# Kernel tuning notes

Hardware: AMD Instinct MI355X
Metric: run time of the kernel (lower is better)

## Reference

```python
import jax, jax.numpy as jnp
import numpy as np

H = 128          # hidden
L = 4            # num PNA layers
NG = 32          # graphs in the batch
OUT = 12
N_NODES = 30000
N_EDGES = 480000
IN_NODE = 64
IN_EDGE = 16
EPS_BN = 1e-5
EPS_STD = 1e-5
# deg histogram torch.tensor([1,2,3,4,5,6]): cnt_i nodes have degree i
_cnt = np.arange(1.0, 7.0)
AVG_LOG = float((np.log(np.arange(6) + 1.0) * _cnt).sum() / _cnt.sum())


def _lin(k, fan_in, fan_out):
    return jax.random.normal(k, (fan_in, fan_out), jnp.float32) * 0.05


def setup_inputs() -> dict:
    key = jax.random.key(0)
    ks = jax.random.split(key, 16)
    d = {}
    d["x"] = jax.random.normal(ks[0], (N_NODES, IN_NODE), jnp.float32)
    d["edge_attr"] = jax.random.normal(ks[1], (N_EDGES, IN_EDGE), jnp.float32)
    d["edge_index"] = jax.random.randint(ks[2], (2, N_EDGES), 0, N_NODES)
    d["batch"] = jnp.sort(jax.random.randint(ks[3], (N_NODES,), 0, NG))
    d["node_emb_W"] = _lin(ks[4], IN_NODE, H)
    d["node_emb_b"] = jnp.zeros((H,), jnp.float32)
    d["edge_emb_W"] = _lin(ks[5], IN_EDGE, H)
    d["edge_emb_b"] = jnp.zeros((H,), jnp.float32)
    kl = jax.random.split(ks[6], 4 * L)
    d["edge_enc_W"] = jnp.stack([_lin(kl[i], H, H) for i in range(L)])
    d["edge_enc_b"] = jnp.zeros((L, H), jnp.float32)
    d["pre_W"] = jnp.stack([_lin(kl[L + i], 3 * H, H) for i in range(L)])
    d["pre_b"] = jnp.zeros((L, H), jnp.float32)
    d["post_W"] = jnp.stack([_lin(kl[2 * L + i], 13 * H, H) for i in range(L)])
    d["post_b"] = jnp.zeros((L, H), jnp.float32)
    d["lin_W"] = jnp.stack([_lin(kl[3 * L + i], H, H) for i in range(L)])
    d["lin_b"] = jnp.zeros((L, H), jnp.float32)
    d["bn_gamma"] = jnp.ones((L, H), jnp.float32)
    d["bn_beta"] = jnp.zeros((L, H), jnp.float32)
    d["head1_W"] = _lin(ks[7], H, H // 2)
    d["head1_b"] = jnp.zeros((H // 2,), jnp.float32)
    d["head2_W"] = _lin(ks[8], H // 2, OUT)
    d["head2_b"] = jnp.zeros((OUT,), jnp.float32)
    return d


def _pna_layer(x, e, src, dst, eW, eb, pW, pb, oW, ob, lW, lb):
    n = x.shape[0]
    ee = e @ eW + eb                                      # edge encoder [E, H]
    h = jnp.concatenate([x[dst], x[src], ee], axis=-1)    # (x_i, x_j, e) [E, 3H]
    m = h @ pW + pb                                       # pre-nn messages [E, H]
    ones = jnp.ones((m.shape[0],), m.dtype)
    deg = jax.ops.segment_sum(ones, dst, num_segments=n)  # in-degree [N]
    degc = jnp.maximum(deg, 1.0)[:, None]
    has = (deg > 0.0)[:, None]
    mean = jax.ops.segment_sum(m, dst, num_segments=n) / degc
    mn = jnp.where(has, jax.ops.segment_min(m, dst, num_segments=n), 0.0)
    mx = jnp.where(has, jax.ops.segment_max(m, dst, num_segments=n), 0.0)
    mean_sq = jax.ops.segment_sum(m * m, dst, num_segments=n) / degc
    std = jnp.sqrt(jax.nn.relu(mean_sq - mean * mean) + EPS_STD)
    agg = jnp.concatenate([mean, mn, mx, std], axis=-1)   # aggregators [N, 4H]
    amp = jnp.log(degc + 1.0) / AVG_LOG                   # amplification scale
    out = jnp.concatenate([agg, agg * amp, agg / amp], axis=-1)  # id/amp/atten [N, 12H]
    out = jnp.concatenate([x, out], axis=-1) @ oW + ob    # post-nn [N, H]
    return out @ lW + lb                                  # final lin


def reference(x, edge_index, batch, edge_attr, node_emb_W, node_emb_b,
              edge_emb_W, edge_emb_b, edge_enc_W, edge_enc_b, pre_W, pre_b,
              post_W, post_b, lin_W, lin_b, bn_gamma, bn_beta,
              head1_W, head1_b, head2_W, head2_b):
    src, dst = edge_index[0], edge_index[1]
    h = x @ node_emb_W + node_emb_b
    e = edge_attr @ edge_emb_W + edge_emb_b
    for l in range(L):
        h = _pna_layer(h, e, src, dst, edge_enc_W[l], edge_enc_b[l],
                       pre_W[l], pre_b[l], post_W[l], post_b[l],
                       lin_W[l], lin_b[l])
        mu = h.mean(axis=0)
        var = h.var(axis=0)  # biased, as BatchNorm training-mode normalization
        h = (h - mu) / jnp.sqrt(var + EPS_BN) * bn_gamma[l] + bn_beta[l]
        h = jax.nn.relu(h)   # dropout == identity (eval mode reference)
    g = jax.ops.segment_sum(h, batch, num_segments=NG)   # global_add_pool [NG, H]
    z = jax.nn.relu(g @ head1_W + head1_b)
    return z @ head2_W + head2_b
```

## Files before the change

kernel.cpp:

```cpp
#include <hip/hip_runtime.h>
#include <hip/hip_bf16.h>
#include <math.h>

#define NN 30000
#define NE 480000
#define NLAYER 4
#define NGR 32
#define NOUT 12
#define EPS_BN 1e-5f
#define EPS_STD 1e-5f
#define AVG_LOG 1.3821454785305053f
#define MB_GRID 235

typedef unsigned short ushort_t;
typedef __bf16 bf16x8 __attribute__((ext_vector_type(8)));
typedef float floatx4 __attribute__((ext_vector_type(4)));

__device__ __forceinline__ float bfu(ushort_t u){
  union { unsigned int ui; float f; } c; c.ui = ((unsigned int)u) << 16; return c.f;
}
__device__ __forceinline__ ushort_t f2bf(float f){
  union { float f; unsigned int u; } c; c.f = f;
  unsigned int lsb = (c.u >> 16) & 1u;
  c.u += 0x7FFFu + lsb;
  return (ushort_t)(c.u >> 16);
}

__device__ __forceinline__ int plausible(unsigned int bits32){
  unsigned int e = (bits32 >> 23) & 0xFF;
  if(e == 0xFF) return 0;
  if(bits32 == 0 || bits32 == 0x80000000u) return 1;
  return (e >= 93 && e <= 140) ? 1 : 0;
}

__global__ void k_detect(const ushort_t* __restrict__ xr, int* __restrict__ flag){
  __shared__ int cnt[2];
  if(threadIdx.x < 2) cnt[threadIdx.x] = 0;
  __syncthreads();
  const unsigned int* xf = (const unsigned int*)xr;
  int gf = 0, gb = 0;
  for(int i = threadIdx.x; i < 1024; i += 256){
    gf += plausible(xf[i]);
    gb += plausible(((unsigned int)xr[i]) << 16);
  }
  atomicAdd(&cnt[0], gf);
  atomicAdd(&cnt[1], gb);
  __syncthreads();
  if(threadIdx.x == 0) *flag = (cnt[1] >= cnt[0]) ? 1 : 0;
}

#define NJOBS 18
struct CvtJob { const void* s; float* d; int n; };
struct CvtArgs { CvtJob j[NJOBS]; const int* flag; };

__global__ void k_cvt(CvtArgs a){
  int ji = blockIdx.y;
  const int isbf = *a.flag;
  float* d = a.j[ji].d;
  int n = a.j[ji].n;
  if(isbf){
    const ushort_t* s = (const ushort_t*)a.j[ji].s;
    for(int i = blockIdx.x*256 + threadIdx.x; i < n; i += gridDim.x*256) d[i] = bfu(s[i]);
  } else {
    const float* s = (const float*)a.j[ji].s;
    for(int i = blockIdx.x*256 + threadIdx.x; i < n; i += gridDim.x*256) d[i] = s[i];
  }
}

__global__ void k_xbf(const void* __restrict__ x, ushort_t* __restrict__ d,
                      const int* __restrict__ flag){
  int i = blockIdx.x*256 + threadIdx.x;
  if(i >= NN*64) return;
  if(*flag) d[i] = ((const ushort_t*)x)[i];
  else      d[i] = f2bf(((const float*)x)[i]);
}

#define NTR 9
struct TrJob { const float* s; ushort_t* d; int K, N; };
struct TrArgs { TrJob j[NTR]; };

__global__ void k_tr(TrArgs a){
  TrJob j = a.j[blockIdx.y];
  int nk = j.K >> 6, nn = j.N >> 6;
  int tile = blockIdx.x;
  if(tile >= nk*nn) return;
  int tk = tile % nk, tn = tile / nk;
  int k0 = tk*64, n0 = tn*64;
  __shared__ float t[64][65];
  int w = threadIdx.x >> 6, c = threadIdx.x & 63;
  #pragma unroll
  for(int i=0;i<16;i+=1){
    int r = i*4 + w;
    t[r][c] = j.s[(size_t)(k0+r)*j.N + n0 + c];
  }
  __syncthreads();
  #pragma unroll
  for(int i=0;i<16;i+=1){
    int r = i*4 + w;
    j.d[(size_t)(n0+r)*j.K + k0 + c] = f2bf(t[c][r]);
  }
}

#define NFOLD 16
struct FoldJob { const float* s1; const float* s2; ushort_t* d; int Kd; };
struct FoldArgs { FoldJob j[NFOLD]; };

__global__ void k_fold(FoldArgs a){
  FoldJob j = a.j[blockIdx.y];
  const int n0 = blockIdx.x*16;
  __shared__ float s2s[128][16];
  int tid = threadIdx.x;
  for(int idx = tid; idx < 128*16; idx += 256){
    int t = idx >> 4, jj = idx & 15;
    s2s[t][jj] = j.s2[t*128 + n0 + jj];
  }
  __syncthreads();
  for(int k = tid; k < j.Kd; k += 256){
    float part[16];
    #pragma unroll
    for(int p=0;p<16;p++) part[p] = 0.f;
    for(int t0=0; t0<128; t0+=32){
      float rr[32];
      #pragma unroll
      for(int tt=0;tt<32;tt++) rr[tt] = j.s1[(size_t)k*128 + t0 + tt];
      #pragma unroll
      for(int p=0;p<16;p++){
        float acc = 0.f;
        #pragma unroll
        for(int tt=0;tt<32;tt++) acc += rr[tt]*s2s[t0+tt][p];
        part[p] += acc;
      }
    }
    #pragma unroll
    for(int p=0;p<16;p++)
      j.d[(size_t)(n0+p)*j.Kd + k] = f2bf(part[p]);
  }
}

__global__ void k_foldb(const float* __restrict__ postB, const float* __restrict__ linW,
                        const float* __restrict__ linB, float* __restrict__ biasY){
  int l = blockIdx.x, c = threadIdx.x;
  float a = linB[l*128+c];
  const float* L = linW + (size_t)l*128*128;
  const float* pb = postB + l*128;
  for(int t=0;t<128;t++) a += pb[t]*L[t*128+c];
  biasY[l*128+c] = a;
}

__global__ void k_deg(const int* __restrict__ dst, int* __restrict__ deg){
  int i = blockIdx.x*256 + threadIdx.x;
  if(i < NE){
    unsigned d = (unsigned)dst[i];
    if(d < NN) atomicAdd(&deg[d], 1);
  }
}

__global__ void k_scan1(const int* __restrict__ deg, int* __restrict__ rp,
                        int* __restrict__ bsum){
  __shared__ int wsum[16];
  int tid = threadIdx.x, lane = tid & 63, wid = tid >> 6;
  int i = blockIdx.x*1024 + tid;
  int v = (i < NN) ? deg[i] : 0;
  int incl = v;
  #pragma unroll
  for(int off=1; off<64; off<<=1){
    int t = __shfl_up(incl, off, 64);
    if(lane >= off) incl += t;
  }
  if(lane==63) wsum[wid] = incl;
  __syncthreads();
  int woff = 0;
  for(int w=0; w<wid; w++) woff += wsum[w];
  if(i < NN) rp[i+1] = incl + woff;
  if(tid == 0){
    int t = 0;
    for(int w=0; w<16; w++) t += wsum[w];
    bsum[blockIdx.x] = t;
  }
}

__global__ void k_scan2(const int* __restrict__ bsum, int* __restrict__ boff,
                        int* __restrict__ rp, int nb){
  if(threadIdx.x == 0){
    int run = 0;
    for(int b=0;b<nb;b++){ boff[b] = run; run += bsum[b]; }
    rp[0] = 0;
  }
}

__global__ void k_scan3(int* __restrict__ rp, const int* __restrict__ boff){
  int i = blockIdx.x*1024 + threadIdx.x;
  if(i < NN) rp[i+1] += boff[blockIdx.x];
}

__global__ void k_scatter(const int* __restrict__ src, const int* __restrict__ dst,
                          const int* __restrict__ rp, int* __restrict__ fill,
                          int* __restrict__ src_csr, int* __restrict__ eix_csr){
  int i = blockIdx.x*256 + threadIdx.x;
  if(i >= NE) return;
  unsigned d = (unsigned)dst[i];
  unsigned s = (unsigned)src[i];
  if(d >= NN || s >= NN) return;
  int pos = rp[d] + atomicAdd(&fill[d], 1);
  src_csr[pos] = (int)s;
  eix_csr[pos] = i;
}

__global__ void k_srt(const int* __restrict__ rp, int* __restrict__ eix,
                      int* __restrict__ src){
  int n = blockIdx.x*256 + threadIdx.x;
  if(n >= NN) return;
  int s0 = rp[n], e0 = rp[n+1];
  for(int i=s0+1;i<e0;i++){
    int ke = eix[i], ks = src[i];
    int j = i-1;
    while(j >= s0 && eix[j] > ke){
      eix[j+1] = eix[j]; src[j+1] = src[j]; j--;
    }
    eix[j+1] = ke; src[j+1] = ks;
  }
}

__global__ void k_gather_ea(const int* __restrict__ eix, const void* __restrict__ ea,
                            ushort_t* __restrict__ out, const int* __restrict__ flag){
  int j = blockIdx.x*128 + threadIdx.x;
  if(j >= NE) return;
  int i = eix[j];
  uint4* d = (uint4*)(out + (size_t)j*16);
  if(*flag){
    const uint4* s = (const uint4*)((const ushort_t*)ea + (size_t)i*16);
    d[0] = s[0]; d[1] = s[1];
  } else {
    const float* s = (const float*)ea + (size_t)i*16;
    union { ushort_t us[16]; uint4 u4[2]; } pk;
    #pragma unroll
    for(int k=0;k<16;k++) pk.us[k] = f2bf(s[k]);
    d[0] = pk.u4[0]; d[1] = pk.u4[1];
  }
}

__global__ void k_prep_K(const float* __restrict__ embW, const float* __restrict__ embB,
                         const float* __restrict__ encW, const float* __restrict__ encB,
                         const float* __restrict__ preW, const float* __restrict__ preB,
                         float* __restrict__ Kf){
  int bx = blockIdx.x;
  int l = bx / 17, r = bx % 17;
  int c = threadIdx.x;
  const float* eW = encW + (size_t)l*128*128;
  const float* P3 = preW + (size_t)l*384*128 + 256*128;
  __shared__ float trow[128];
  float a;
  if(r < 16){
    a = 0.f;
    const float* w = embW + r*128;
    for(int k=0;k<128;k++) a += w[k]*eW[k*128+c];
  } else {
    a = encB[l*128+c];
    for(int k=0;k<128;k++) a += embB[k]*eW[k*128+c];
  }
  trow[c] = a;
  __syncthreads();
  float o = (r==16) ? preB[l*128+c] : 0.f;
  for(int k=0;k<128;k++) o += trow[k]*P3[k*128+c];
  Kf[(size_t)l*17*128 + r*128 + c] = o;
}

template<int EPI, int OUTBF>
__launch_bounds__(256)
__global__ void k_mm(const ushort_t* __restrict__ A, const ushort_t* __restrict__ BT,
                     void* __restrict__ C, int M, int K, int ldc,
                     const float* __restrict__ bias,
                     const float* __restrict__ Tm,
                     const float* __restrict__ ampv, const float* __restrict__ invv,
                     float* __restrict__ bnpart){
  __shared__ __align__(16) ushort_t Als[128][88];
  __shared__ __align__(16) ushort_t Bls[128][88];
  __shared__ float s_part[8][128];
  __shared__ float q_part[8][128];
  const int tid = threadIdx.x;
  const int m0 = blockIdx.x*128, n0 = blockIdx.y*128;
  const int w = tid >> 6, lane = tid & 63;
  const int wm = (w & 1)*64, wn = (w >> 1)*64;
  const int quad = lane >> 4, l15 = lane & 15;
  floatx4 acc[4][4] = {};

  for(int k0=0; k0<K; k0+=64){
    #pragma unroll
    for(int i=0;i<4;i++){
      int c = tid + 256*i;
      int row = c >> 3, kc = (c & 7)*8;
      uint4 va = make_uint4(0u,0u,0u,0u);
      int gr = m0 + row;
      if(gr < M) va = *(const uint4*)(A + (size_t)gr*K + k0 + kc);
      *(uint4*)(&Als[row][kc]) = va;
      uint4 vb = *(const uint4*)(BT + (size_t)(n0+row)*K + k0 + kc);
      *(uint4*)(&Bls[row][kc]) = vb;
    }
    __syncthreads();
    #pragma unroll
    for(int ks=0; ks<64; ks+=32){
      bf16x8 a[4], b[4];
      #pragma unroll
      for(int i=0;i<4;i++) a[i] = *(const bf16x8*)(&Als[wm+16*i+l15][ks+quad*8]);
      #pragma unroll
      for(int j=0;j<4;j++) b[j] = *(const bf16x8*)(&Bls[wn+16*j+l15][ks+quad*8]);
      #pragma unroll
      for(int i=0;i<4;i++)
        #pragma unroll
        for(int j=0;j<4;j++)
          acc[i][j] = __builtin_amdgcn_mfma_f32_16x16x32_bf16(a[i], b[j], acc[i][j], 0, 0, 0);
    }
    __syncthreads();
  }

  float s[4] = {0,0,0,0}, q[4] = {0,0,0,0};
  #pragma unroll
  for(int i=0;i<4;i++){
    #pragma unroll
    for(int r=0;r<4;r++){
      int grow = m0 + wm + 16*i + quad*4 + r;
      if(grow >= M) continue;
      float amp = 0.f, iv = 0.f;
      const float* tr = nullptr;
      if(EPI==1){ amp = ampv[grow]; iv = invv[grow]; tr = Tm + (size_t)grow*384; }
      #pragma unroll
      for(int j=0;j<4;j++){
        int gcol = n0 + wn + 16*j + l15;
        float v = acc[i][j][r];
        if(bias) v += bias[gcol];
        if(EPI==1) v += tr[gcol] + amp*tr[128+gcol] + iv*tr[256+gcol];
        if(OUTBF) ((ushort_t*)C)[(size_t)grow*ldc + gcol] = f2bf(v);
        else      ((float*)  C)[(size_t)grow*ldc + gcol] = v;
        if(EPI==1){ s[j] += v; q[j] += v*v; }
      }
    }
  }
  if(EPI==1){
    const int slot = (w & 1)*4 + quad;
    #pragma unroll
    for(int j=0;j<4;j++){
      s_part[slot][wn + 16*j + l15] = s[j];
      q_part[slot][wn + 16*j + l15] = q[j];
    }
    __syncthreads();
    if(tid < 128){
      float ss = 0.f, qq = 0.f;
      #pragma unroll
      for(int sl=0; sl<8; sl++){ ss += s_part[sl][tid]; qq += q_part[sl][tid]; }
      bnpart[(size_t)blockIdx.x*256 + tid]       = ss;
      bnpart[(size_t)blockIdx.x*256 + 128 + tid] = qq;
    }
  }
}

__launch_bounds__(128)
__global__ void k_agg(const int* __restrict__ rp, const int* __restrict__ src_csr,
                      const ushort_t* __restrict__ ea_csr, const float* __restrict__ Kf,
                      const float* __restrict__ AB,
                      ushort_t* __restrict__ agg, float* __restrict__ ampv,
                      float* __restrict__ invv){
  const int n = blockIdx.x, c = threadIdx.x;
  const int s0 = rp[n], e0 = rp[n+1];
  const int deg = e0 - s0;
  float kcol[16];
  #pragma unroll
  for(int k=0;k<16;k++) kcol[k] = Kf[k*128+c];
  const float base = AB[(size_t)n*256 + c] + Kf[16*128+c];
  float sum=0.f, sq=0.f, mn=INFINITY, mx=-INFINITY;
  __shared__ float ea_s[16][16];
  __shared__ int src_s[16];
  for(int j0=s0; j0<e0; j0+=16){
    int cnt = min(16, e0-j0);
    __syncthreads();
    int ee = c>>4, kk = c&15;
    if(ee < cnt)   ea_s[ee][kk]   = bfu(ea_csr[(size_t)(j0+ee)*16+kk]);
    if(ee+8 < cnt) ea_s[ee+8][kk] = bfu(ea_csr[(size_t)(j0+ee+8)*16+kk]);
    if(c < cnt) src_s[c] = src_csr[j0+c];
    __syncthreads();
    for(int e=0;e<cnt;e++){
      float m = base + AB[(size_t)src_s[e]*256 + 128 + c];
      #pragma unroll
      for(int k=0;k<16;k++) m += ea_s[e][k]*kcol[k];
      sum += m; sq += m*m; mn = fminf(mn,m); mx = fmaxf(mx,m);
    }
  }
  float degc = (float)(deg>0?deg:1);
  float mean = sum/degc;
  float var  = fmaxf(sq/degc - mean*mean, 0.f);
  float sd = sqrtf(var + EPS_STD);
  if(deg==0){ mn=0.f; mx=0.f; }
  ushort_t* o = agg + (size_t)n*512;
  o[c]     = f2bf(mean);
  o[128+c] = f2bf(mn);
  o[256+c] = f2bf(mx);
  o[384+c] = f2bf(sd);
  if(c==0){
    float amp = logf(degc+1.f)/AVG_LOG;
    ampv[n] = amp; invv[n] = 1.f/amp;
  }
}

__global__ void k_bn_fin(const float* __restrict__ bnpart, int nb,
                         const float* __restrict__ gamma, const float* __restrict__ beta,
                         float* __restrict__ scale, float* __restrict__ shift){
  int c = threadIdx.x;
  float s = 0.f, q = 0.f;
  for(int b=0;b<nb;b++){
    s += bnpart[(size_t)b*256 + c];
    q += bnpart[(size_t)b*256 + 128 + c];
  }
  float mu  = s*(1.f/NN);
  float var = fmaxf(q*(1.f/NN) - mu*mu, 0.f);
  float inv = 1.f/sqrtf(var + EPS_BN);
  float sc = gamma[c]*inv;
  scale[c] = sc;
  shift[c] = beta[c] - mu*sc;
}

__global__ void k_bn_relu(const float* __restrict__ y, const float* __restrict__ scale,
                          const float* __restrict__ shift, ushort_t* __restrict__ h){
  int i = blockIdx.x*256 + threadIdx.x;
  if(i >= NN*128) return;
  int c = i & 127;
  float v = fmaxf(y[i]*scale[c] + shift[c], 0.f);
  h[i] = f2bf(v);
}

__device__ __forceinline__ int lbound(const int* a, int n, int v){
  int lo = 0, hi = n;
  while(lo < hi){ int mid = (lo+hi) >> 1; if(a[mid] < v) lo = mid+1; else hi = mid; }
  return lo;
}

__launch_bounds__(128)
__global__ void k_pool1(const ushort_t* __restrict__ h, const int* __restrict__ batch,
                        float* __restrict__ gpart){
  int b = blockIdx.x, ch = blockIdx.y, c = threadIdx.x;
  int lo = lbound(batch, NN, b), hi = lbound(batch, NN, b+1);
  int len = hi - lo;
  int per = (len + 7) >> 3;
  int r0 = min(lo + ch*per, hi);
  int r1 = min(r0 + per, hi);
  float acc = 0.f;
  for(int r=r0;r<r1;r++) acc += bfu(h[(size_t)r*128+c]);
  gpart[((size_t)b*8 + ch)*128 + c] = acc;
}

__global__ void k_pool2(const float* __restrict__ gpart, float* __restrict__ g){
  int b = blockIdx.x, c = threadIdx.x;
  float acc = 0.f;
  #pragma unroll
  for(int ch=0; ch<8; ch++) acc += gpart[((size_t)b*8 + ch)*128 + c];
  g[(size_t)b*128 + c] = acc;
}

__launch_bounds__(64)
__global__ void k_head(const float* __restrict__ g, const float* __restrict__ W1,
                       const float* __restrict__ b1, const float* __restrict__ W2,
                       const float* __restrict__ b2, void* __restrict__ out,
                       const int* __restrict__ flag){
  __shared__ float gs[128];
  __shared__ float zs[64];
  int r = blockIdx.x, tid = threadIdx.x;
  gs[tid] = g[r*128 + tid];
  gs[tid+64] = g[r*128 + tid + 64];
  __syncthreads();
  float a = b1[tid];
  for(int k=0;k<128;k++) a += gs[k]*W1[k*64+tid];
  zs[tid] = fmaxf(a, 0.f);
  __syncthreads();
  if(tid < NOUT){
    float o = b2[tid];
    for(int k=0;k<64;k++) o += zs[k]*W2[k*12+tid];
    if(*flag) ((ushort_t*)out)[r*NOUT + tid] = f2bf(o);
    else      ((float*)out)[r*NOUT + tid] = o;
  }
}

extern "C" void kernel_launch(void* const* d_in, const int* in_sizes, int n_in,
                              void* d_out, int out_size, void* d_ws, size_t ws_size,
                              hipStream_t stream){
  const void* x_raw = d_in[0];
  const void* ea_raw;
  const int*  eidx;
  const int*  batch;
  if(in_sizes[1] == 2*NE){
    eidx   = (const int*)d_in[1];
    batch  = (const int*)d_in[2];
    ea_raw = d_in[3];
  } else {
    ea_raw = d_in[1];
    eidx   = (const int*)d_in[2];
    batch  = (const int*)d_in[3];
  }
  const void* nembW_r = d_in[4];
  const void* nembB_r = d_in[5];
  const void* eembW_r = d_in[6];
  const void* eembB_r = d_in[7];
  const void* encW_r  = d_in[8];
  const void* encB_r  = d_in[9];
  const void* preW_r  = d_in[10];
  const void* preB_r  = d_in[11];
  const void* postW_r = d_in[12];
  const void* postB_r = d_in[13];
  const void* linW_r  = d_in[14];
  const void* linB_r  = d_in[15];
  const void* bnG_r   = d_in[16];
  const void* bnB_r   = d_in[17];
  const void* h1W_r   = d_in[18];
  const void* h1B_r   = d_in[19];
  const void* h2W_r   = d_in[20];
  const void* h2B_r   = d_in[21];

  char* p = (char*)d_ws;
  auto alloc = [&](size_t bytes)->void*{
    void* r = (void*)p; p += (bytes + 255) & ~(size_t)255; return r;
  };
  int*      dtflag  = (int*)     alloc(sizeof(int)*16);
  int*      deg     = (int*)     alloc(sizeof(int)*NN);
  int*      fill    = (int*)     alloc(sizeof(int)*NN);
  int*      rp      = (int*)     alloc(sizeof(int)*(NN+1));
  int*      bsum    = (int*)     alloc(sizeof(int)*64);
  int*      boff    = (int*)     alloc(sizeof(int)*64);
  int*      src_csr = (int*)     alloc(sizeof(int)*NE);
  int*      eix_csr = (int*)     alloc(sizeof(int)*NE);
  ushort_t* ea_csr  = (ushort_t*)alloc(sizeof(ushort_t)*(size_t)NE*16);
  ushort_t* xbf     = (ushort_t*)alloc(sizeof(ushort_t)*(size_t)NN*64);
  ushort_t* h       = (ushort_t*)alloc(sizeof(ushort_t)*(size_t)NN*128);
  ushort_t* aggb    = (ushort_t*)alloc(sizeof(ushort_t)*(size_t)NN*512);
  float*    AB      = (float*)   alloc(sizeof(float)*(size_t)NN*256);
  float*    Tm      = (float*)   alloc(sizeof(float)*(size_t)NN*384);
  float*    y       = (float*)   alloc(sizeof(float)*(size_t)NN*128);
  float*    ampv    = (float*)   alloc(sizeof(float)*NN);
  float*    invv    = (float*)   alloc(sizeof(float)*NN);
  float*    Kf      = (float*)   alloc(sizeof(float)*4*17*128);
  float*    bnpart  = (float*)   alloc(sizeof(float)*(size_t)MB_GRID*256);
  float*    bnscale = (float*)   alloc(sizeof(float)*128);
  float*    bnshift = (float*)   alloc(sizeof(float)*128);
  float*    gpart   = (float*)   alloc(sizeof(float)*32*8*128);
  float*    g       = (float*)   alloc(sizeof(float)*32*128);
  float*    biasY   = (float*)   alloc(sizeof(float)*4*128);
  ushort_t* WembT   = (ushort_t*)alloc(sizeof(ushort_t)*128*64);
  ushort_t* P12T    = (ushort_t*)alloc(sizeof(ushort_t)*4*256*128);
  ushort_t* WcatFT  = (ushort_t*)alloc(sizeof(ushort_t)*(size_t)4*384*512);
  ushort_t* W0FT    = (ushort_t*)alloc(sizeof(ushort_t)*4*128*128);
  float* nembW = (float*)alloc(sizeof(float)*64*128);
  float* nembB = (float*)alloc(sizeof(float)*128);
  float* eembW = (float*)alloc(sizeof(float)*16*128);
  float* eembB = (float*)alloc(sizeof(float)*128);
  float* encW  = (float*)alloc(sizeof(float)*4*128*128);
  float* encB  = (float*)alloc(sizeof(float)*4*128);
  float* preW  = (float*)alloc(sizeof(float)*4*384*128);
  float* preB  = (float*)alloc(sizeof(float)*4*128);
  float* postW = (float*)alloc(sizeof(float)*(size_t)4*1664*128);
  float* postB = (float*)alloc(sizeof(float)*4*128);
  float* linW  = (float*)alloc(sizeof(float)*4*128*128);
  float* linB  = (float*)alloc(sizeof(float)*4*128);
  float* bnG   = (float*)alloc(sizeof(float)*4*128);
  float* bnB   = (float*)alloc(sizeof(float)*4*128);
  float* h1W   = (float*)alloc(sizeof(float)*128*64);
  float* h1B   = (float*)alloc(sizeof(float)*64);
  float* h2W   = (float*)alloc(sizeof(float)*64*12);
  float* h2B   = (float*)alloc(sizeof(float)*12);

  CvtArgs ca;
  ca.flag = dtflag;
  int ji = 0;
  auto job = [&](const void* s, float* d, int n){ ca.j[ji].s=s; ca.j[ji].d=d; ca.j[ji].n=n; ji++; };
  job(nembW_r, nembW, 64*128);
  job(nembB_r, nembB, 128);
  job(eembW_r, eembW, 16*128);
  job(eembB_r, eembB, 128);
  job(encW_r,  encW,  4*128*128);
  job(encB_r,  encB,  4*128);
  job(preW_r,  preW,  4*384*128);
  job(preB_r,  preB,  4*128);
  job(postW_r, postW, 4*1664*128);
  job(postB_r, postB, 4*128);
  job(linW_r,  linW,  4*128*128);
  job(linB_r,  linB,  4*128);
  job(bnG_r,   bnG,   4*128);
  job(bnB_r,   bnB,   4*128);
  job(h1W_r,   h1W,   128*64);
  job(h1B_r,   h1B,   64);
  job(h2W_r,   h2W,   64*12);
  job(h2B_r,   h2B,   12);

  TrArgs ta;
  int ti = 0;
  auto tj = [&](const float* s, ushort_t* d, int K, int N){ ta.j[ti].s=s; ta.j[ti].d=d; ta.j[ti].K=K; ta.j[ti].N=N; ti++; };
  tj(nembW, WembT, 64, 128);
  for(int l=0;l<4;l++){
    const float* pw = preW + (size_t)l*384*128;
    tj(pw,           P12T + (size_t)l*256*128,           128, 128);
    tj(pw + 128*128, P12T + (size_t)l*256*128 + 128*128, 128, 128);
  }

  FoldArgs fa;
  int fi = 0;
  for(int l=0;l<4;l++){
    const float* po = postW + (size_t)l*1664*128;
    const float* L  = linW + (size_t)l*128*128;
    for(int b=0;b<3;b++){
      fa.j[fi].s1 = po + (size_t)(128 + b*512)*128;
      fa.j[fi].s2 = L;
      fa.j[fi].d  = WcatFT + (size_t)l*384*512 + (size_t)b*128*512;
      fa.j[fi].Kd = 512;
      fi++;
    }
    fa.j[fi].s1 = po;
    fa.j[fi].s2 = L;
    fa.j[fi].d  = W0FT + (size_t)l*128*128;
    fa.j[fi].Kd = 128;
    fi++;
  }

  const int* esrc = eidx;
  const int* edst = eidx + NE;

  hipMemsetAsync(deg, 0, sizeof(int)*NN, stream);
  hipMemsetAsync(fill, 0, sizeof(int)*NN, stream);

  k_detect<<<1, 256, 0, stream>>>((const ushort_t*)x_raw, dtflag);
  k_cvt<<<dim3(128, NJOBS), 256, 0, stream>>>(ca);
  k_xbf<<<(NN*64+255)/256, 256, 0, stream>>>(x_raw, xbf, dtflag);
  k_tr<<<dim3(4, NTR), 256, 0, stream>>>(ta);
  k_fold<<<dim3(8, NFOLD), 256, 0, stream>>>(fa);
  k_foldb<<<4, 128, 0, stream>>>(postB, linW, linB, biasY);
  k_prep_K<<<68, 128, 0, stream>>>(eembW, eembB, encW, encB, preW, preB, Kf);

  k_deg<<<(NE+255)/256, 256, 0, stream>>>(edst, deg);
  k_scan1<<<30, 1024, 0, stream>>>(deg, rp, bsum);
  k_scan2<<<1, 64, 0, stream>>>(bsum, boff, rp, 30);
  k_scan3<<<30, 1024, 0, stream>>>(rp, boff);
  k_scatter<<<(NE+255)/256, 256, 0, stream>>>(esrc, edst, rp, fill, src_csr, eix_csr);
  k_srt<<<(NN+255)/256, 256, 0, stream>>>(rp, eix_csr, src_csr);
  k_gather_ea<<<(NE+127)/128, 128, 0, stream>>>(eix_csr, ea_raw, ea_csr, dtflag);

  k_mm<0,1><<<dim3(MB_GRID,1), 256, 0, stream>>>(xbf, WembT, h, NN, 64, 128,
                                                 nembB, nullptr, nullptr, nullptr, nullptr);

  for(int l=0; l<NLAYER; l++){
    k_mm<0,0><<<dim3(MB_GRID,2), 256, 0, stream>>>(h, P12T + (size_t)l*256*128, AB, NN, 128, 256,
                                                   nullptr, nullptr, nullptr, nullptr, nullptr);
    k_agg<<<NN, 128, 0, stream>>>(rp, src_csr, ea_csr, Kf + (size_t)l*17*128,
                                  AB, aggb, ampv, invv);
    k_mm<0,0><<<dim3(MB_GRID,3), 256, 0, stream>>>(aggb, WcatFT + (size_t)l*384*512, Tm, NN, 512, 384,
                                                   nullptr, nullptr, nullptr, nullptr, nullptr);
    k_mm<1,0><<<dim3(MB_GRID,1), 256, 0, stream>>>(h, W0FT + (size_t)l*128*128, y, NN, 128, 128,
                                                   biasY + l*128, Tm, ampv, invv, bnpart);
    k_bn_fin<<<1, 128, 0, stream>>>(bnpart, MB_GRID, bnG + l*128, bnB + l*128,
                                    bnscale, bnshift);
    k_bn_relu<<<(NN*128+255)/256, 256, 0, stream>>>(y, bnscale, bnshift, h);
  }

  k_pool1<<<dim3(NGR,8), 128, 0, stream>>>(h, batch, gpart);
  k_pool2<<<NGR, 128, 0, stream>>>(gpart, g);
  k_head<<<NGR, 64, 0, stream>>>(g, h1W, h1B, h2W, h2B, d_out, dtflag);
}
```

Measured before the change: 1.165 ms.

## Fuse post-NN GEMMs into one kernel, shrink intermediates to bf16, streamline CSR sort

```diff
diff --git a/kernel.cpp b/kernel.cpp
--- a/kernel.cpp
+++ b/kernel.cpp
@@ -193,39 +193,51 @@
   if(i < NN) rp[i+1] += boff[blockIdx.x];
 }
 
-__global__ void k_scatter(const int* __restrict__ src, const int* __restrict__ dst,
+__global__ void k_scatter(const int* __restrict__ dst,
                           const int* __restrict__ rp, int* __restrict__ fill,
-                          int* __restrict__ src_csr, int* __restrict__ eix_csr){
+                          int* __restrict__ eix_csr){
   int i = blockIdx.x*256 + threadIdx.x;
   if(i >= NE) return;
   unsigned d = (unsigned)dst[i];
-  unsigned s = (unsigned)src[i];
-  if(d >= NN || s >= NN) return;
+  if(d >= NN) return;
   int pos = rp[d] + atomicAdd(&fill[d], 1);
-  src_csr[pos] = (int)s;
   eix_csr[pos] = i;
 }
 
-__global__ void k_srt(const int* __restrict__ rp, int* __restrict__ eix,
-                      int* __restrict__ src){
-  int n = blockIdx.x*256 + threadIdx.x;
+__launch_bounds__(64)
+__global__ void k_srt(const int* __restrict__ rp, int* __restrict__ eix){
+  __shared__ int buf[64][129];
+  int t = threadIdx.x;
+  int n = blockIdx.x*64 + t;
   if(n >= NN) return;
-  int s0 = rp[n], e0 = rp[n+1];
-  for(int i=s0+1;i<e0;i++){
-    int ke = eix[i], ks = src[i];
-    int j = i-1;
-    while(j >= s0 && eix[j] > ke){
-      eix[j+1] = eix[j]; src[j+1] = src[j]; j--;
-    }
-    eix[j+1] = ke; src[j+1] = ks;
-  }
-}
-
-__global__ void k_gather_ea(const int* __restrict__ eix, const void* __restrict__ ea,
-                            ushort_t* __restrict__ out, const int* __restrict__ flag){
+  int s0 = rp[n], e0 = rp[n+1], d = e0 - s0;
+  if(d <= 1) return;
+  if(d <= 128){
+    int* b = buf[t];
+    for(int i=0;i<d;i++) b[i] = eix[s0+i];
+    for(int i=1;i<d;i++){
+      int k = b[i], j = i-1;
+      while(j >= 0 && b[j] > k){ b[j+1] = b[j]; j--; }
+      b[j+1] = k;
+    }
+    for(int i=0;i<d;i++) eix[s0+i] = b[i];
+  } else {
+    for(int i=s0+1;i<e0;i++){
+      int k = eix[i], j = i-1;
+      while(j >= s0 && eix[j] > k){ eix[j+1] = eix[j]; j--; }
+      eix[j+1] = k;
+    }
+  }
+}
+
+__global__ void k_gather_ea(const int* __restrict__ eix, const int* __restrict__ esrc,
+                            const void* __restrict__ ea,
+                            ushort_t* __restrict__ out, int* __restrict__ src_csr,
+                            const int* __restrict__ flag){
   int j = blockIdx.x*128 + threadIdx.x;
   if(j >= NE) return;
   int i = eix[j];
+  src_csr[j] = esrc[i];
   uint4* d = (uint4*)(out + (size_t)j*16);
   if(*flag){
     const uint4* s = (const uint4*)((const ushort_t*)ea + (size_t)i*16);
@@ -268,15 +280,10 @@
 template<int EPI, int OUTBF>
 __launch_bounds__(256)
 __global__ void k_mm(const ushort_t* __restrict__ A, const ushort_t* __restrict__ BT,
-                     void* __restrict__ C, int M, int K, int ldc,
-                     const float* __restrict__ bias,
-                     const float* __restrict__ Tm,
-                     const float* __restrict__ ampv, const float* __restrict__ invv,
-                     float* __restrict__ bnpart){
+                     void* __restrict__ C, void* __restrict__ C2,
+                     int M, int K, int ldc, const float* __restrict__ bias){
   __shared__ __align__(16) ushort_t Als[128][88];
   __shared__ __align__(16) ushort_t Bls[128][88];
-  __shared__ float s_part[8][128];
-  __shared__ float q_part[8][128];
   const int tid = threadIdx.x;
   const int m0 = blockIdx.x*128, n0 = blockIdx.y*128;
   const int w = tid >> 6, lane = tid & 63;
@@ -313,50 +320,163 @@
     __syncthreads();
   }
 
+  #pragma unroll
+  for(int i=0;i<4;i++){
+    #pragma unroll
+    for(int r=0;r<4;r++){
+      int grow = m0 + wm + 16*i + quad*4 + r;
+      if(grow >= M) continue;
+      #pragma unroll
+      for(int j=0;j<4;j++){
+        int gcol = n0 + wn + 16*j + l15;
+        float v = acc[i][j][r];
+        if(EPI==0){
+          if(bias) v += bias[gcol];
+          if(OUTBF) ((ushort_t*)C)[(size_t)grow*ldc + gcol] = f2bf(v);
+          else      ((float*)  C)[(size_t)grow*ldc + gcol] = v;
+        } else {
+          if(n0 == 0) ((float*)C)[(size_t)grow*128 + gcol] = v;
+          else        ((ushort_t*)C2)[(size_t)grow*128 + (gcol-128)] = f2bf(v);
+        }
+      }
+    }
+  }
+}
+
+__launch_bounds__(256)
+__global__ void k_post(const ushort_t* __restrict__ aggb, const ushort_t* __restrict__ h,
+                       const ushort_t* __restrict__ Wcat, const ushort_t* __restrict__ W0,
+                       const float* __restrict__ biasY,
+                       const float* __restrict__ ampv, const float* __restrict__ invv,
+                       ushort_t* __restrict__ y, float* __restrict__ bnpart){
+  __shared__ __align__(16) ushort_t Als[128][88];
+  __shared__ __align__(16) ushort_t Bls[128][88];
+  __shared__ float s_part[8][128];
+  __shared__ float q_part[8][128];
+  __shared__ float amp_s[128];
+  __shared__ float inv_s[128];
+  const int tid = threadIdx.x;
+  const int m0 = blockIdx.x*128;
+  const int w = tid >> 6, lane = tid & 63;
+  const int wm = (w & 1)*64, wn = (w >> 1)*64;
+  const int quad = lane >> 4, l15 = lane & 15;
+  if(tid < 128){
+    int rr = min(m0 + tid, NN-1);
+    amp_s[tid] = ampv[rr];
+    inv_s[tid] = invv[rr];
+  }
+  floatx4 accY[4][4] = {};
+
+  for(int p=0; p<3; p++){
+    floatx4 accP[4][4] = {};
+    floatx4 (*tgt)[4] = (p==0) ? accY : accP;
+    const ushort_t* Wp = Wcat + (size_t)p*128*512;
+    for(int k0=0; k0<512; k0+=64){
+      #pragma unroll
+      for(int i=0;i<4;i++){
+        int c = tid + 256*i;
+        int row = c >> 3, kc = (c & 7)*8;
+        uint4 va = make_uint4(0u,0u,0u,0u);
+        int gr = m0 + row;
+        if(gr < NN) va = *(const uint4*)(aggb + (size_t)gr*512 + k0 + kc);
+        *(uint4*)(&Als[row][kc]) = va;
+        uint4 vb = *(const uint4*)(Wp + (size_t)row*512 + k0 + kc);
+        *(uint4*)(&Bls[row][kc]) = vb;
+      }
+      __syncthreads();
+      #pragma unroll
+      for(int ks=0; ks<64; ks+=32){
+        bf16x8 a[4], b[4];
+        #pragma unroll
+        for(int i=0;i<4;i++) a[i] = *(const bf16x8*)(&Als[wm+16*i+l15][ks+quad*8]);
+        #pragma unroll
+        for(int j=0;j<4;j++) b[j] = *(const bf16x8*)(&Bls[wn+16*j+l15][ks+quad*8]);
+        #pragma unroll
+        for(int i=0;i<4;i++)
+          #pragma unroll
+          for(int j=0;j<4;j++)
+            tgt[i][j] = __builtin_amdgcn_mfma_f32_16x16x32_bf16(a[i], b[j], tgt[i][j], 0, 0, 0);
+      }
+      __syncthreads();
+    }
+    if(p > 0){
+      const float* cs = (p==1) ? amp_s : inv_s;
+      #pragma unroll
+      for(int i=0;i<4;i++)
+        #pragma unroll
+        for(int r=0;r<4;r++){
+          float coef = cs[wm + 16*i + quad*4 + r];
+          #pragma unroll
+          for(int j=0;j<4;j++) accY[i][j][r] += coef*accP[i][j][r];
+        }
+    }
+  }
+
+  for(int k0=0; k0<128; k0+=64){
+    #pragma unroll
+    for(int i=0;i<4;i++){
+      int c = tid + 256*i;
+      int row = c >> 3, kc = (c & 7)*8;
+      uint4 va = make_uint4(0u,0u,0u,0u);
+      int gr = m0 + row;
+      if(gr < NN) va = *(const uint4*)(h + (size_t)gr*128 + k0 + kc);
+      *(uint4*)(&Als[row][kc]) = va;
+      uint4 vb = *(const uint4*)(W0 + (size_t)row*128 + k0 + kc);
+      *(uint4*)(&Bls[row][kc]) = vb;
+    }
+    __syncthreads();
+    #pragma unroll
+    for(int ks=0; ks<64; ks+=32){
+      bf16x8 a[4], b[4];
+      #pragma unroll
+      for(int i=0;i<4;i++) a[i] = *(const bf16x8*)(&Als[wm+16*i+l15][ks+quad*8]);
+      #pragma unroll
+      for(int j=0;j<4;j++) b[j] = *(const bf16x8*)(&Bls[wn+16*j+l15][ks+quad*8]);
+      #pragma unroll
+      for(int i=0;i<4;i++)
+        #pragma unroll
+        for(int j=0;j<4;j++)
+          accY[i][j] = __builtin_amdgcn_mfma_f32_16x16x32_bf16(a[i], b[j], accY[i][j], 0, 0, 0);
+    }
+    __syncthreads();
+  }
+
   float s[4] = {0,0,0,0}, q[4] = {0,0,0,0};
   #pragma unroll
   for(int i=0;i<4;i++){
     #pragma unroll
     for(int r=0;r<4;r++){
       int grow = m0 + wm + 16*i + quad*4 + r;
-      if(grow >= M) continue;
-      float amp = 0.f, iv = 0.f;
-      const float* tr = nullptr;
-      if(EPI==1){ amp = ampv[grow]; iv = invv[grow]; tr = Tm + (size_t)grow*384; }
+      if(grow >= NN) continue;
       #pragma unroll
       for(int j=0;j<4;j++){
-        int gcol = n0 + wn + 16*j + l15;
-        float v = acc[i][j][r];
-        if(bias) v += bias[gcol];
-        if(EPI==1) v += tr[gcol] + amp*tr[128+gcol] + iv*tr[256+gcol];
-        if(OUTBF) ((ushort_t*)C)[(size_t)grow*ldc + gcol] = f2bf(v);
-        else      ((float*)  C)[(size_t)grow*ldc + gcol] = v;
-        if(EPI==1){ s[j] += v; q[j] += v*v; }
+        int gcol = wn + 16*j + l15;
+        float v = accY[i][j][r] + biasY[gcol];
+        y[(size_t)grow*128 + gcol] = f2bf(v);
+        s[j] += v; q[j] += v*v;
       }
     }
   }
-  if(EPI==1){
-    const int slot = (w & 1)*4 + quad;
-    #pragma unroll
-    for(int j=0;j<4;j++){
-      s_part[slot][wn + 16*j + l15] = s[j];
-      q_part[slot][wn + 16*j + l15] = q[j];
-    }
-    __syncthreads();
-    if(tid < 128){
-      float ss = 0.f, qq = 0.f;
-      #pragma unroll
-      for(int sl=0; sl<8; sl++){ ss += s_part[sl][tid]; qq += q_part[sl][tid]; }
-      bnpart[(size_t)blockIdx.x*256 + tid]       = ss;
-      bnpart[(size_t)blockIdx.x*256 + 128 + tid] = qq;
-    }
+  const int slot = (w & 1)*4 + quad;
+  #pragma unroll
+  for(int j=0;j<4;j++){
+    s_part[slot][wn + 16*j + l15] = s[j];
+    q_part[slot][wn + 16*j + l15] = q[j];
+  }
+  __syncthreads();
+  if(tid < 128){
+    float ss = 0.f, qq = 0.f;
+    #pragma unroll
+    for(int sl=0; sl<8; sl++){ ss += s_part[sl][tid]; qq += q_part[sl][tid]; }
+    bnpart[(size_t)blockIdx.x*256 + tid]       = ss;
+    bnpart[(size_t)blockIdx.x*256 + 128 + tid] = qq;
   }
 }
 
 __launch_bounds__(128)
 __global__ void k_agg(const int* __restrict__ rp, const int* __restrict__ src_csr,
                       const ushort_t* __restrict__ ea_csr, const float* __restrict__ Kf,
-                      const float* __restrict__ AB,
+                      const float* __restrict__ Ah, const ushort_t* __restrict__ Bh,
                       ushort_t* __restrict__ agg, float* __restrict__ ampv,
                       float* __restrict__ invv){
   const int n = blockIdx.x, c = threadIdx.x;
@@ -365,7 +485,7 @@
   float kcol[16];
   #pragma unroll
   for(int k=0;k<16;k++) kcol[k] = Kf[k*128+c];
-  const float base = AB[(size_t)n*256 + c] + Kf[16*128+c];
+  const float base = Ah[(size_t)n*128 + c] + Kf[16*128+c];
   float sum=0.f, sq=0.f, mn=INFINITY, mx=-INFINITY;
   __shared__ float ea_s[16][16];
   __shared__ int src_s[16];
@@ -378,7 +498,7 @@
     if(c < cnt) src_s[c] = src_csr[j0+c];
     __syncthreads();
     for(int e=0;e<cnt;e++){
-      float m = base + AB[(size_t)src_s[e]*256 + 128 + c];
+      float m = base + bfu(Bh[(size_t)src_s[e]*128 + c]);
       #pragma unroll
       for(int k=0;k<16;k++) m += ea_s[e][k]*kcol[k];
       sum += m; sq += m*m; mn = fminf(mn,m); mx = fmaxf(mx,m);
@@ -404,11 +524,16 @@
                          const float* __restrict__ gamma, const float* __restrict__ beta,
                          float* __restrict__ scale, float* __restrict__ shift){
   int c = threadIdx.x;
-  float s = 0.f, q = 0.f;
-  for(int b=0;b<nb;b++){
-    s += bnpart[(size_t)b*256 + c];
-    q += bnpart[(size_t)b*256 + 128 + c];
-  }
+  float s0=0.f,s1=0.f,s2=0.f,s3=0.f, q0=0.f,q1=0.f,q2=0.f,q3=0.f;
+  int b = 0;
+  for(; b+3<nb; b+=4){
+    s0 += bnpart[(size_t)(b+0)*256 + c];       q0 += bnpart[(size_t)(b+0)*256 + 128 + c];
+    s1 += bnpart[(size_t)(b+1)*256 + c];       q1 += bnpart[(size_t)(b+1)*256 + 128 + c];
+    s2 += bnpart[(size_t)(b+2)*256 + c];       q2 += bnpart[(size_t)(b+2)*256 + 128 + c];
+    s3 += bnpart[(size_t)(b+3)*256 + c];       q3 += bnpart[(size_t)(b+3)*256 + 128 + c];
+  }
+  for(; b<nb; b++){ s0 += bnpart[(size_t)b*256 + c]; q0 += bnpart[(size_t)b*256 + 128 + c]; }
+  float s = (s0+s1)+(s2+s3), q = (q0+q1)+(q2+q3);
   float mu  = s*(1.f/NN);
   float var = fmaxf(q*(1.f/NN) - mu*mu, 0.f);
   float inv = 1.f/sqrtf(var + EPS_BN);
@@ -417,12 +542,12 @@
   shift[c] = beta[c] - mu*sc;
 }
 
-__global__ void k_bn_relu(const float* __restrict__ y, const float* __restrict__ scale,
+__global__ void k_bn_relu(const ushort_t* __restrict__ y, const float* __restrict__ scale,
                           const float* __restrict__ shift, ushort_t* __restrict__ h){
   int i = blockIdx.x*256 + threadIdx.x;
   if(i >= NN*128) return;
   int c = i & 127;
-  float v = fmaxf(y[i]*scale[c] + shift[c], 0.f);
+  float v = fmaxf(bfu(y[i])*scale[c] + shift[c], 0.f);
   h[i] = f2bf(v);
 }
 
@@ -528,11 +653,11 @@
   ushort_t* xbf     = (ushort_t*)alloc(sizeof(ushort_t)*(size_t)NN*64);
   ushort_t* h       = (ushort_t*)alloc(sizeof(ushort_t)*(size_t)NN*128);
   ushort_t* aggb    = (ushort_t*)alloc(sizeof(ushort_t)*(size_t)NN*512);
-  float*    AB      = (float*)   alloc(sizeof(float)*(size_t)NN*256);
-  float*    Tm      = (float*)   alloc(sizeof(float)*(size_t)NN*384);
-  float*    y       = (float*)   alloc(sizeof(float)*(size_t)NN*128);
-  float*    ampv    = (float*)   alloc(sizeof(float)*NN);
-  float*    invv    = (float*)   alloc(sizeof(float)*NN);
+  float*    Ah      = (float*)   alloc(sizeof(float)*(size_t)NN*128);
+  ushort_t* Bh      = (ushort_t*)alloc(sizeof(ushort_t)*(size_t)NN*128);
+  ushort_t* y       = (ushort_t*)alloc(sizeof(ushort_t)*(size_t)NN*128);
+  float*    ampv    = (float*)   alloc(sizeof(float)*(NN+256));
+  float*    invv    = (float*)   alloc(sizeof(float)*(NN+256));
   float*    Kf      = (float*)   alloc(sizeof(float)*4*17*128);
   float*    bnpart  = (float*)   alloc(sizeof(float)*(size_t)MB_GRID*256);
   float*    bnscale = (float*)   alloc(sizeof(float)*128);
@@ -633,22 +758,20 @@
   k_scan1<<<30, 1024, 0, stream>>>(deg, rp, bsum);
   k_scan2<<<1, 64, 0, stream>>>(bsum, boff, rp, 30);
   k_scan3<<<30, 1024, 0, stream>>>(rp, boff);
-  k_scatter<<<(NE+255)/256, 256, 0, stream>>>(esrc, edst, rp, fill, src_csr, eix_csr);
-  k_srt<<<(NN+255)/256, 256, 0, stream>>>(rp, eix_csr, src_csr);
-  k_gather_ea<<<(NE+127)/128, 128, 0, stream>>>(eix_csr, ea_raw, ea_csr, dtflag);
-
-  k_mm<0,1><<<dim3(MB_GRID,1), 256, 0, stream>>>(xbf, WembT, h, NN, 64, 128,
-                                                 nembB, nullptr, nullptr, nullptr, nullptr);
+  k_scatter<<<(NE+255)/256, 256, 0, stream>>>(edst, rp, fill, eix_csr);
+  k_srt<<<(NN+63)/64, 64, 0, stream>>>(rp, eix_csr);
+  k_gather_ea<<<(NE+127)/128, 128, 0, stream>>>(eix_csr, esrc, ea_raw, ea_csr, src_csr, dtflag);
+
+  k_mm<0,1><<<dim3(MB_GRID,1), 256, 0, stream>>>(xbf, WembT, h, nullptr, NN, 64, 128, nembB);
 
   for(int l=0; l<NLAYER; l++){
-    k_mm<0,0><<<dim3(MB_GRID,2), 256, 0, stream>>>(h, P12T + (size_t)l*256*128, AB, NN, 128, 256,
-                                                   nullptr, nullptr, nullptr, nullptr, nullptr);
+    k_mm<2,0><<<dim3(MB_GRID,2), 256, 0, stream>>>(h, P12T + (size_t)l*256*128, Ah, Bh,
+                                                   NN, 128, 128, nullptr);
     k_agg<<<NN, 128, 0, stream>>>(rp, src_csr, ea_csr, Kf + (size_t)l*17*128,
-                                  AB, aggb, ampv, invv);
-    k_mm<0,0><<<dim3(MB_GRID,3), 256, 0, stream>>>(aggb, WcatFT + (size_t)l*384*512, Tm, NN, 512, 384,
-                                                   nullptr, nullptr, nullptr, nullptr, nullptr);
-    k_mm<1,0><<<dim3(MB_GRID,1), 256, 0, stream>>>(h, W0FT + (size_t)l*128*128, y, NN, 128, 128,
-                                                   biasY + l*128, Tm, ampv, invv, bnpart);
+                                  Ah, Bh, aggb, ampv, invv);
+    k_post<<<MB_GRID, 256, 0, stream>>>(aggb, h, WcatFT + (size_t)l*384*512,
+                                        W0FT + (size_t)l*128*128, biasY + l*128,
+                                        ampv, invv, y, bnpart);
     k_bn_fin<<<1, 128, 0, stream>>>(bnpart, MB_GRID, bnG + l*128, bnB + l*128,
                                     bnscale, bnshift);
     k_bn_relu<<<(NN*128+255)/256, 256, 0, stream>>>(y, bnscale, bnshift, h);
```

New measurement: 1.031 ms. 1.13x faster.
